# Kernel tuning notes

Measured on AMD Instinct MI355X. Metric: run time of the kernel, lower is better.

## Reference

```python
import jax, jax.numpy as jnp
import numpy as np

N = 100000          # total nodes
F = 128             # in_features
B = 1000            # number of graphs
NPG = 100           # nodes per graph (contiguous)
DEG = 16            # avg degree
E = B * NPG * DEG   # total edges (intra-graph)
K_RATIO = 0.8
KNUM = max(1, int(K_RATIO * NPG))  # nodes kept per graph = 80


def setup_inputs() -> dict:
    key = jax.random.key(0)
    k1, k2, k3, k4 = jax.random.split(key, 4)
    x = jax.random.normal(k1, (N, F), dtype=jnp.float32)
    # intra-graph random edges: offset each block of NPG*DEG edges by its graph's base node id
    offs = (jnp.arange(E, dtype=jnp.int32) // (NPG * DEG)) * NPG
    src = jax.random.randint(k2, (E,), 0, NPG, dtype=jnp.int32) + offs
    dst = jax.random.randint(k3, (E,), 0, NPG, dtype=jnp.int32) + offs
    edge_index = jnp.stack([src, dst], axis=0)
    batch = (jnp.arange(N, dtype=jnp.int32) // NPG).astype(jnp.int32)
    limit = float(np.sqrt(6.0 / (F + 1)))  # xavier_uniform for (F,1)
    theta_att = jax.random.uniform(k4, (F, 1), dtype=jnp.float32, minval=-limit, maxval=limit)
    return {"x": x, "edge_index": edge_index, "batch": batch, "theta_att": theta_att}


def reference(x, edge_index, batch, theta_att):
    num_nodes = x.shape[0]
    # add self loops with weight 1
    loops = jnp.arange(num_nodes, dtype=edge_index.dtype)
    row = jnp.concatenate([edge_index[0], loops])
    col = jnp.concatenate([edge_index[1], loops])
    w = jnp.ones(row.shape[0], dtype=x.dtype)
    # symmetric degree normalization (degree counted over row, as in torch code)
    deg = jax.ops.segment_sum(w, row, num_segments=num_nodes)
    dis = jnp.where(deg > 0, jax.lax.rsqrt(deg), jnp.zeros((), x.dtype))
    norm = dis[row] * w * dis[col]
    # scatter-add: agg[dst] += x[src] * norm
    agg = jax.ops.segment_sum(x[row] * norm[:, None], col, num_segments=num_nodes)
    z = (agg @ theta_att)[:, 0]                     # (N,)
    # per-graph top-k: graphs are contiguous and equal-sized -> reshape
    zb = z.reshape(B, NPG)
    _, pos = jax.lax.top_k(zb, KNUM)                # (B, KNUM) positions within each graph
    pos = jnp.sort(pos, axis=1)                     # global sort of keep_idx == per-graph sort here
    keep = (pos + jnp.arange(B, dtype=pos.dtype)[:, None] * NPG).reshape(-1)  # (B*KNUM,)
    scale = jax.nn.sigmoid(z[keep])[:, None]
    x_new = x[keep] * scale                         # (B*KNUM, F)
    batch_new = batch[keep]
    # subgraph with relabeled nodes; dropped edges padded with -1 (fixed shape for jit)
    node_mask = jnp.zeros(num_nodes, dtype=bool).at[keep].set(True)
    new_id = jnp.cumsum(node_mask.astype(jnp.int32)) - 1
    emask = node_mask[edge_index[0]] & node_mask[edge_index[1]]
    edge_index_new = jnp.where(emask[None, :], new_id[edge_index], -1)
    return x_new, edge_index_new, batch_new
```

## Files before the change

kernel.cpp:

```cpp
#include <hip/hip_runtime.h>


#define NPG   100
#define EPG   1600
#define KNUM  80
#define FDIM  128
#define BT    512
#define NF4   (NPG * FDIM / 4)
#define NE4   (EPG / 4)
#define NCH   (NF4 / BT)
#define PSTR  33

__global__ __launch_bounds__(BT)
void sagpool_fused6(const float* __restrict__ x,
                    const int*   __restrict__ ei,
                    const float* __restrict__ theta,
                    float* __restrict__ out,
                    int E_total, int out_x_elems)
{
    const int g    = blockIdx.x;
    const int tid  = threadIdx.x;
    const int wave = tid >> 6;
    const int lane = tid & 63;
    const int base = g * NPG;

    __shared__ int4   sh_edge4[NE4];
    __shared__ int    sh_cnt[8][NPG];
    __shared__ double sh_part[NPG * PSTR];
    __shared__ double sh_dis[NPG];
    __shared__ double sh_a[NPG];
    __shared__ double sh_zp[8][NPG];
    __shared__ double sh_z[NPG];
    __shared__ unsigned long long sh_mask7[8];
    __shared__ int    sh_newid[NPG];
    __shared__ float  sh_scalen[NPG];
    int* sh_edge = (int*)sh_edge4;

    {
        int*    cw = sh_cnt[wave];
        double* zw = sh_zp[wave];
        for (int i = lane; i < NPG; i += 64) { cw[i] = 0; zw[i] = 0.0; }
    }

    const float4 th = ((const float4*)theta)[lane & 31];

    const int4* src4 = (const int4*)(ei + (size_t)g * EPG);
    const int4* dst4 = (const int4*)(ei + (size_t)E_total + (size_t)g * EPG);
    const bool  hasE = tid < NE4;
    int4 es, ed;
    if (hasE) { es = src4[tid]; ed = dst4[tid]; }

    const float4* xb4 = (const float4*)(x + (size_t)base * FDIM);
    float4 v[NCH];
    #pragma unroll
    for (int i = 0; i < NCH; ++i) v[i] = xb4[i * BT + tid];
    const bool hasR = tid < (NF4 - NCH * BT);
    float4 vR;
    if (hasR) vR = xb4[NCH * BT + tid];

    if (hasE) {
        int4 s4 = es, d4 = ed;
        s4.x -= base; s4.y -= base; s4.z -= base; s4.w -= base;
        d4.x -= base; d4.y -= base; d4.z -= base; d4.w -= base;
        int4 p; p.x = s4.x | (d4.x << 16); p.y = s4.y | (d4.y << 16);
                p.z = s4.z | (d4.z << 16); p.w = s4.w | (d4.w << 16);
        sh_edge4[tid] = p;
        int* cw = sh_cnt[wave];
        atomicAdd(&cw[s4.x], 1); atomicAdd(&cw[s4.y], 1);
        atomicAdd(&cw[s4.z], 1); atomicAdd(&cw[s4.w], 1);
    }

    #pragma unroll
    for (int i = 0; i < NCH; ++i) {
        int idx = i * BT + tid;
        double p = (double)v[i].x * th.x + (double)v[i].y * th.y
                 + (double)v[i].z * th.z + (double)v[i].w * th.w;
        sh_part[idx + (idx >> 5)] = p;
    }
    if (hasR) {
        int idx = NCH * BT + tid;
        double p = (double)vR.x * th.x + (double)vR.y * th.y
                 + (double)vR.z * th.z + (double)vR.w * th.w;
        sh_part[idx + (idx >> 5)] = p;
    }
    __syncthreads();

    if (tid < 4 * NPG) {
        const int n = tid >> 2, q = tid & 3;
        const double* pr = sh_part + n * PSTR + q * 8;
        double s = ((pr[0] + pr[1]) + (pr[2] + pr[3]))
                 + ((pr[4] + pr[5]) + (pr[6] + pr[7]));
        s += __shfl_xor(s, 1, 64);
        s += __shfl_xor(s, 2, 64);
        if (q == 0) {
            int deg = 1 + sh_cnt[0][n] + sh_cnt[1][n] + sh_cnt[2][n]
                        + sh_cnt[3][n] + sh_cnt[4][n] + sh_cnt[5][n]
                        + sh_cnt[6][n] + sh_cnt[7][n];
            double dis = 1.0 / sqrt((double)deg);
            sh_dis[n] = dis;
            sh_a[n]   = s * dis;
        }
    }
    __syncthreads();

    {
        double* zp = sh_zp[wave];
        for (int j = tid; j < EPG; j += BT) {
            int p = sh_edge[j];
            int s = p & 0xffff;
            int d = p >> 16;
            atomicAdd(&zp[d], sh_a[s]);
        }
    }
    __syncthreads();

    if (tid < NPG) {
        double zi = sh_a[tid]
                  + sh_zp[0][tid] + sh_zp[1][tid] + sh_zp[2][tid] + sh_zp[3][tid]
                  + sh_zp[4][tid] + sh_zp[5][tid] + sh_zp[6][tid] + sh_zp[7][tid];
        sh_z[tid] = zi * sh_dis[tid];
        sh_newid[tid] = -1;
    }
    __syncthreads();

    const bool rk = tid < 4 * NPG;
    const int  n  = tid >> 2;
    int r = 0;
    double zn = 0.0;
    if (rk) {
        zn = sh_z[n];
        const int j0 = (tid & 3) * 25;
        for (int j = j0; j < j0 + 25; ++j) {
            double zj = sh_z[j];
            r += (int)((zj > zn) | ((zj == zn) & (j < n)));
        }
    }
    r += __shfl_xor(r, 1, 64);
    r += __shfl_xor(r, 2, 64);
    const bool lead = rk && ((tid & 3) == 0) && (r < KNUM);
    unsigned long long m = __ballot(lead);
    if (lane == 0) sh_mask7[wave] = m;
    __syncthreads();

    if (lead) {
        int before = __popcll(m & ((1ull << lane) - 1ull));
        for (int w2 = 0; w2 < wave; ++w2) before += __popcll(sh_mask7[w2]);
        int row = g * KNUM + before;
        sh_newid[n]  = row;
        float zf = (float)zn;
        sh_scalen[n] = 1.0f / (1.0f + __expf(-zf));
        out[(size_t)out_x_elems + 2 * (size_t)E_total + row] = (float)g;
    }
    __syncthreads();

    float4* outx = (float4*)out;
    #pragma unroll
    for (int i = 0; i < NCH; ++i) {
        int idx = i * BT + tid;
        int row = idx >> 5;
        int nid = sh_newid[row];
        if (nid >= 0) {
            float sc = sh_scalen[row];
            float4 o;
            o.x = v[i].x * sc; o.y = v[i].y * sc;
            o.z = v[i].z * sc; o.w = v[i].w * sc;
            outx[(size_t)nid * 32 + (idx & 31)] = o;
        }
    }
    if (hasR) {
        int idx = NCH * BT + tid;
        int row = idx >> 5;
        int nid = sh_newid[row];
        if (nid >= 0) {
            float sc = sh_scalen[row];
            float4 o;
            o.x = vR.x * sc; o.y = vR.y * sc;
            o.z = vR.z * sc; o.w = vR.w * sc;
            outx[(size_t)nid * 32 + (idx & 31)] = o;
        }
    }

    float* e0 = out + out_x_elems;
    float* e1 = e0 + E_total;
    if (hasE) {
        int4 p = sh_edge4[tid];
        float4 o0, o1;
        {
            int s = p.x & 0xffff, d = p.x >> 16;
            int a = sh_newid[s], b = sh_newid[d];
            bool vv = (a >= 0) && (b >= 0);
            o0.x = vv ? (float)a : -1.0f; o1.x = vv ? (float)b : -1.0f;
        }
        {
            int s = p.y & 0xffff, d = p.y >> 16;
            int a = sh_newid[s], b = sh_newid[d];
            bool vv = (a >= 0) && (b >= 0);
            o0.y = vv ? (float)a : -1.0f; o1.y = vv ? (float)b : -1.0f;
        }
        {
            int s = p.z & 0xffff, d = p.z >> 16;
            int a = sh_newid[s], b = sh_newid[d];
            bool vv = (a >= 0) && (b >= 0);
            o0.z = vv ? (float)a : -1.0f; o1.z = vv ? (float)b : -1.0f;
        }
        {
            int s = p.w & 0xffff, d = p.w >> 16;
            int a = sh_newid[s], b = sh_newid[d];
            bool vv = (a >= 0) && (b >= 0);
            o0.w = vv ? (float)a : -1.0f; o1.w = vv ? (float)b : -1.0f;
        }
        ((float4*)e0)[(size_t)g * NE4 + tid] = o0;
        ((float4*)e1)[(size_t)g * NE4 + tid] = o1;
    }
}

extern "C" void kernel_launch(void* const* d_in, const int* in_sizes, int n_in,
                              void* d_out, int out_size, void* d_ws, size_t ws_size,
                              hipStream_t stream)
{
    const float* x     = (const float*)d_in[0];
    const int*   ei    = (const int*)d_in[1];
    const float* theta = (const float*)d_in[3];
    float* out = (float*)d_out;

    const int N = in_sizes[0] / FDIM;
    const int E = in_sizes[1] / 2;
    const int B = N / NPG;
    const int out_x_elems = B * KNUM * FDIM;

    sagpool_fused6<<<dim3(B), dim3(BT), 0, stream>>>(x, ei, theta, out, E, out_x_elems);
}
```

Baseline: 114.3 us.

## Process two graphs per block and prefetch the second graph's data early

Moves the per-graph body into a device function and has each block handle two consecutive graphs. Both graphs' node features and edges are loaded into registers at kernel start, so the second graph's global loads can overlap the first graph's reduction, top-k and output phases. The cost is half as many blocks, more registers per thread, and the second graph running serially after the first within the block. A min-blocks hint is added to launch bounds.

```diff
diff --git a/kernel.cpp b/kernel.cpp
--- a/kernel.cpp
+++ b/kernel.cpp
@@ -6,66 +6,51 @@
 #define KNUM  80
 #define FDIM  128
 #define BT    512
+#define GPB   2
 #define NF4   (NPG * FDIM / 4)
 #define NE4   (EPG / 4)
 #define NCH   (NF4 / BT)
+#define NREM  (NF4 - NCH * BT)
 #define PSTR  33
 
-__global__ __launch_bounds__(BT)
-void sagpool_fused6(const float* __restrict__ x,
-                    const int*   __restrict__ ei,
-                    const float* __restrict__ theta,
-                    float* __restrict__ out,
-                    int E_total, int out_x_elems)
+struct Smem {
+    int4   edge4[NE4];
+    int    cnt[8][NPG];
+    double part[NPG * PSTR];
+    double dis[NPG];
+    double a[NPG];
+    double zp[8][NPG];
+    double z[NPG];
+    unsigned long long mask7[8];
+    int    newid[NPG];
+    float  scalen[NPG];
+};
+
+__device__ __forceinline__
+void process_graph(Smem& sm, int g, int tid, int wave, int lane, float4 th,
+                   const float4 (&v)[NCH], float4 vR, int4 es, int4 ed,
+                   float* __restrict__ out, int E_total, int out_x_elems)
 {
-    const int g    = blockIdx.x;
-    const int tid  = threadIdx.x;
-    const int wave = tid >> 6;
-    const int lane = tid & 63;
-    const int base = g * NPG;
-
-    __shared__ int4   sh_edge4[NE4];
-    __shared__ int    sh_cnt[8][NPG];
-    __shared__ double sh_part[NPG * PSTR];
-    __shared__ double sh_dis[NPG];
-    __shared__ double sh_a[NPG];
-    __shared__ double sh_zp[8][NPG];
-    __shared__ double sh_z[NPG];
-    __shared__ unsigned long long sh_mask7[8];
-    __shared__ int    sh_newid[NPG];
-    __shared__ float  sh_scalen[NPG];
-    int* sh_edge = (int*)sh_edge4;
+    const int  base = g * NPG;
+    const bool hasE = tid < NE4;
+    const bool hasR = tid < NREM;
+    int* sh_edge = (int*)sm.edge4;
 
     {
-        int*    cw = sh_cnt[wave];
-        double* zw = sh_zp[wave];
+        int*    cw = sm.cnt[wave];
+        double* zw = sm.zp[wave];
         for (int i = lane; i < NPG; i += 64) { cw[i] = 0; zw[i] = 0.0; }
     }
 
-    const float4 th = ((const float4*)theta)[lane & 31];
-
-    const int4* src4 = (const int4*)(ei + (size_t)g * EPG);
-    const int4* dst4 = (const int4*)(ei + (size_t)E_total + (size_t)g * EPG);
-    const bool  hasE = tid < NE4;
-    int4 es, ed;
-    if (hasE) { es = src4[tid]; ed = dst4[tid]; }
-
-    const float4* xb4 = (const float4*)(x + (size_t)base * FDIM);
-    float4 v[NCH];
-    #pragma unroll
-    for (int i = 0; i < NCH; ++i) v[i] = xb4[i * BT + tid];
-    const bool hasR = tid < (NF4 - NCH * BT);
-    float4 vR;
-    if (hasR) vR = xb4[NCH * BT + tid];
-
+    int4 p;
     if (hasE) {
         int4 s4 = es, d4 = ed;
         s4.x -= base; s4.y -= base; s4.z -= base; s4.w -= base;
         d4.x -= base; d4.y -= base; d4.z -= base; d4.w -= base;
-        int4 p; p.x = s4.x | (d4.x << 16); p.y = s4.y | (d4.y << 16);
-                p.z = s4.z | (d4.z << 16); p.w = s4.w | (d4.w << 16);
-        sh_edge4[tid] = p;
-        int* cw = sh_cnt[wave];
+        p.x = s4.x | (d4.x << 16); p.y = s4.y | (d4.y << 16);
+        p.z = s4.z | (d4.z << 16); p.w = s4.w | (d4.w << 16);
+        sm.edge4[tid] = p;
+        int* cw = sm.cnt[wave];
         atomicAdd(&cw[s4.x], 1); atomicAdd(&cw[s4.y], 1);
         atomicAdd(&cw[s4.z], 1); atomicAdd(&cw[s4.w], 1);
     }
@@ -73,82 +58,79 @@
     #pragma unroll
     for (int i = 0; i < NCH; ++i) {
         int idx = i * BT + tid;
-        double p = (double)v[i].x * th.x + (double)v[i].y * th.y
-                 + (double)v[i].z * th.z + (double)v[i].w * th.w;
-        sh_part[idx + (idx >> 5)] = p;
+        double dp = (double)v[i].x * th.x + (double)v[i].y * th.y
+                  + (double)v[i].z * th.z + (double)v[i].w * th.w;
+        sm.part[idx + (idx >> 5)] = dp;
     }
     if (hasR) {
         int idx = NCH * BT + tid;
-        double p = (double)vR.x * th.x + (double)vR.y * th.y
-                 + (double)vR.z * th.z + (double)vR.w * th.w;
-        sh_part[idx + (idx >> 5)] = p;
+        double dp = (double)vR.x * th.x + (double)vR.y * th.y
+                  + (double)vR.z * th.z + (double)vR.w * th.w;
+        sm.part[idx + (idx >> 5)] = dp;
     }
     __syncthreads();
 
     if (tid < 4 * NPG) {
         const int n = tid >> 2, q = tid & 3;
-        const double* pr = sh_part + n * PSTR + q * 8;
+        const double* pr = sm.part + n * PSTR + q * 8;
         double s = ((pr[0] + pr[1]) + (pr[2] + pr[3]))
                  + ((pr[4] + pr[5]) + (pr[6] + pr[7]));
         s += __shfl_xor(s, 1, 64);
         s += __shfl_xor(s, 2, 64);
         if (q == 0) {
-            int deg = 1 + sh_cnt[0][n] + sh_cnt[1][n] + sh_cnt[2][n]
-                        + sh_cnt[3][n] + sh_cnt[4][n] + sh_cnt[5][n]
-                        + sh_cnt[6][n] + sh_cnt[7][n];
+            int deg = 1 + sm.cnt[0][n] + sm.cnt[1][n] + sm.cnt[2][n]
+                        + sm.cnt[3][n] + sm.cnt[4][n] + sm.cnt[5][n]
+                        + sm.cnt[6][n] + sm.cnt[7][n];
             double dis = 1.0 / sqrt((double)deg);
-            sh_dis[n] = dis;
-            sh_a[n]   = s * dis;
+            sm.dis[n] = dis;
+            sm.a[n]   = s * dis;
         }
     }
     __syncthreads();
 
     {
-        double* zp = sh_zp[wave];
+        double* zw = sm.zp[wave];
         for (int j = tid; j < EPG; j += BT) {
-            int p = sh_edge[j];
-            int s = p & 0xffff;
-            int d = p >> 16;
-            atomicAdd(&zp[d], sh_a[s]);
+            int e = sh_edge[j];
+            atomicAdd(&zw[e >> 16], sm.a[e & 0xffff]);
         }
     }
     __syncthreads();
 
     if (tid < NPG) {
-        double zi = sh_a[tid]
-                  + sh_zp[0][tid] + sh_zp[1][tid] + sh_zp[2][tid] + sh_zp[3][tid]
-                  + sh_zp[4][tid] + sh_zp[5][tid] + sh_zp[6][tid] + sh_zp[7][tid];
-        sh_z[tid] = zi * sh_dis[tid];
-        sh_newid[tid] = -1;
+        double zi = sm.a[tid]
+                  + sm.zp[0][tid] + sm.zp[1][tid] + sm.zp[2][tid] + sm.zp[3][tid]
+                  + sm.zp[4][tid] + sm.zp[5][tid] + sm.zp[6][tid] + sm.zp[7][tid];
+        sm.z[tid] = zi * sm.dis[tid];
+        sm.newid[tid] = -1;
     }
     __syncthreads();
 
     const bool rk = tid < 4 * NPG;
-    const int  n  = tid >> 2;
+    const int  n2 = tid >> 2;
     int r = 0;
     double zn = 0.0;
     if (rk) {
-        zn = sh_z[n];
+        zn = sm.z[n2];
         const int j0 = (tid & 3) * 25;
         for (int j = j0; j < j0 + 25; ++j) {
-            double zj = sh_z[j];
-            r += (int)((zj > zn) | ((zj == zn) & (j < n)));
+            double zj = sm.z[j];
+            r += (int)((zj > zn) | ((zj == zn) & (j < n2)));
         }
     }
     r += __shfl_xor(r, 1, 64);
     r += __shfl_xor(r, 2, 64);
     const bool lead = rk && ((tid & 3) == 0) && (r < KNUM);
     unsigned long long m = __ballot(lead);
-    if (lane == 0) sh_mask7[wave] = m;
+    if (lane == 0) sm.mask7[wave] = m;
     __syncthreads();
 
     if (lead) {
         int before = __popcll(m & ((1ull << lane) - 1ull));
-        for (int w2 = 0; w2 < wave; ++w2) before += __popcll(sh_mask7[w2]);
+        for (int w2 = 0; w2 < wave; ++w2) before += __popcll(sm.mask7[w2]);
         int row = g * KNUM + before;
-        sh_newid[n]  = row;
-        float zf = (float)zn;
-        sh_scalen[n] = 1.0f / (1.0f + __expf(-zf));
+        sm.newid[n2]  = row;
+        sm.scalen[n2] = 1.0f / (1.0f + __expf(-(float)zn));
         out[(size_t)out_x_elems + 2 * (size_t)E_total + row] = (float)g;
     }
     __syncthreads();
@@ -157,10 +139,9 @@
     #pragma unroll
     for (int i = 0; i < NCH; ++i) {
         int idx = i * BT + tid;
-        int row = idx >> 5;
-        int nid = sh_newid[row];
+        int nid = sm.newid[idx >> 5];
         if (nid >= 0) {
-            float sc = sh_scalen[row];
+            float sc = sm.scalen[idx >> 5];
             float4 o;
             o.x = v[i].x * sc; o.y = v[i].y * sc;
             o.z = v[i].z * sc; o.w = v[i].w * sc;
@@ -169,10 +150,9 @@
     }
     if (hasR) {
         int idx = NCH * BT + tid;
-        int row = idx >> 5;
-        int nid = sh_newid[row];
+        int nid = sm.newid[idx >> 5];
         if (nid >= 0) {
-            float sc = sh_scalen[row];
+            float sc = sm.scalen[idx >> 5];
             float4 o;
             o.x = vR.x * sc; o.y = vR.y * sc;
             o.z = vR.z * sc; o.w = vR.w * sc;
@@ -183,35 +163,80 @@
     float* e0 = out + out_x_elems;
     float* e1 = e0 + E_total;
     if (hasE) {
-        int4 p = sh_edge4[tid];
         float4 o0, o1;
         {
-            int s = p.x & 0xffff, d = p.x >> 16;
-            int a = sh_newid[s], b = sh_newid[d];
-            bool vv = (a >= 0) && (b >= 0);
-            o0.x = vv ? (float)a : -1.0f; o1.x = vv ? (float)b : -1.0f;
-        }
-        {
-            int s = p.y & 0xffff, d = p.y >> 16;
-            int a = sh_newid[s], b = sh_newid[d];
-            bool vv = (a >= 0) && (b >= 0);
-            o0.y = vv ? (float)a : -1.0f; o1.y = vv ? (float)b : -1.0f;
-        }
-        {
-            int s = p.z & 0xffff, d = p.z >> 16;
-            int a = sh_newid[s], b = sh_newid[d];
-            bool vv = (a >= 0) && (b >= 0);
-            o0.z = vv ? (float)a : -1.0f; o1.z = vv ? (float)b : -1.0f;
-        }
-        {
-            int s = p.w & 0xffff, d = p.w >> 16;
-            int a = sh_newid[s], b = sh_newid[d];
-            bool vv = (a >= 0) && (b >= 0);
-            o0.w = vv ? (float)a : -1.0f; o1.w = vv ? (float)b : -1.0f;
+            int a_ = sm.newid[p.x & 0xffff], b_ = sm.newid[p.x >> 16];
+            bool vv = (a_ >= 0) && (b_ >= 0);
+            o0.x = vv ? (float)a_ : -1.0f; o1.x = vv ? (float)b_ : -1.0f;
+        }
+        {
+            int a_ = sm.newid[p.y & 0xffff], b_ = sm.newid[p.y >> 16];
+            bool vv = (a_ >= 0) && (b_ >= 0);
+            o0.y = vv ? (float)a_ : -1.0f; o1.y = vv ? (float)b_ : -1.0f;
+        }
+        {
+            int a_ = sm.newid[p.z & 0xffff], b_ = sm.newid[p.z >> 16];
+            bool vv = (a_ >= 0) && (b_ >= 0);
+            o0.z = vv ? (float)a_ : -1.0f; o1.z = vv ? (float)b_ : -1.0f;
+        }
+        {
+            int a_ = sm.newid[p.w & 0xffff], b_ = sm.newid[p.w >> 16];
+            bool vv = (a_ >= 0) && (b_ >= 0);
+            o0.w = vv ? (float)a_ : -1.0f; o1.w = vv ? (float)b_ : -1.0f;
         }
         ((float4*)e0)[(size_t)g * NE4 + tid] = o0;
         ((float4*)e1)[(size_t)g * NE4 + tid] = o1;
     }
+}
+
+__global__ __launch_bounds__(BT, 4)
+void sagpool_fused7(const float* __restrict__ x,
+                    const int*   __restrict__ ei,
+                    const float* __restrict__ theta,
+                    float* __restrict__ out,
+                    int E_total, int out_x_elems, int n_graphs)
+{
+    __shared__ Smem sm;
+    const int tid  = threadIdx.x;
+    const int wave = tid >> 6;
+    const int lane = tid & 63;
+    const int gA   = blockIdx.x * GPB;
+    const int gB   = gA + 1;
+    const bool hasE = tid < NE4;
+    const bool hasR = tid < NREM;
+
+    const float4 th = ((const float4*)theta)[lane & 31];
+
+    int4 esA, edA, esB, edB;
+    float4 vA[NCH], vB[NCH], vRA, vRB;
+
+    if (hasE) {
+        esA = ((const int4*)(ei + (size_t)gA * EPG))[tid];
+        edA = ((const int4*)(ei + (size_t)E_total + (size_t)gA * EPG))[tid];
+    }
+    {
+        const float4* xb4 = (const float4*)(x + (size_t)gA * NPG * FDIM);
+        #pragma unroll
+        for (int i = 0; i < NCH; ++i) vA[i] = xb4[i * BT + tid];
+        if (hasR) vRA = xb4[NCH * BT + tid];
+    }
+    const bool doB = gB < n_graphs;
+    if (doB) {
+        if (hasE) {
+            esB = ((const int4*)(ei + (size_t)gB * EPG))[tid];
+            edB = ((const int4*)(ei + (size_t)E_total + (size_t)gB * EPG))[tid];
+        }
+        const float4* xb4 = (const float4*)(x + (size_t)gB * NPG * FDIM);
+        #pragma unroll
+        for (int i = 0; i < NCH; ++i) vB[i] = xb4[i * BT + tid];
+        if (hasR) vRB = xb4[NCH * BT + tid];
+    }
+
+    process_graph(sm, gA, tid, wave, lane, th, vA, vRA, esA, edA,
+                  out, E_total, out_x_elems);
+    if (doB)
+        process_graph(sm, gB, tid, wave, lane, th, vB, vRB, esB, edB,
+                      out, E_total, out_x_elems);
 }
 
 extern "C" void kernel_launch(void* const* d_in, const int* in_sizes, int n_in,
@@ -227,6 +252,8 @@
     const int E = in_sizes[1] / 2;
     const int B = N / NPG;
     const int out_x_elems = B * KNUM * FDIM;
-
-    sagpool_fused6<<<dim3(B), dim3(BT), 0, stream>>>(x, ei, theta, out, E, out_x_elems);
+    const int nb = (B + GPB - 1) / GPB;
+
+    sagpool_fused7<<<dim3(nb), dim3(BT), 0, stream>>>(x, ei, theta, out,
+                                                      E, out_x_elems, B);
 }
```

Result: slower. 129.7 us (+13.4%).
